# Kernel optimization log

Measured on AMD Instinct MI355X. Metric: run time of the kernel, lower is better.

The kernel has to match this reference:

```python
import jax, jax.numpy as jnp
import numpy as np

N = 60000      # total nodes
D = 300        # feature dim
R = 5          # num relations == num bases
E = 1_000_000  # edges
S = 25000      # last_idx_senses
G = 50000      # last_idx_globals
BATCH = 32


def setup_inputs() -> dict:
    key = jax.random.key(0)
    ks = jax.random.split(key, 12)
    x = jax.random.normal(ks[0], (N, D), dtype=jnp.float32)
    edge_index = jax.random.randint(ks[1], (2, E), 0, N, dtype=jnp.int32)
    edge_type = jax.random.randint(ks[2], (E,), 0, R, dtype=jnp.int32)
    current_node_index = jax.random.randint(ks[3], (BATCH,), 0, N, dtype=jnp.int32)
    scale = 1.0 / np.sqrt(D)
    # RGCNConv basis decomposition params (num_bases == num_relations)
    basis = jax.random.normal(ks[4], (R, D, D), dtype=jnp.float32) * scale
    comp = jax.random.normal(ks[5], (R, R), dtype=jnp.float32) * scale
    root = jax.random.normal(ks[6], (D, D), dtype=jnp.float32) * scale
    bias = jnp.zeros((D,), dtype=jnp.float32)
    # heads
    w_global = jax.random.normal(ks[7], (G - S, D), dtype=jnp.float32) * scale
    b_global = jnp.zeros((G - S,), dtype=jnp.float32)
    w_sense = jax.random.normal(ks[8], (S, D), dtype=jnp.float32) * scale
    b_sense = jnp.zeros((S,), dtype=jnp.float32)
    return {
        "x": x, "edge_index": edge_index, "edge_type": edge_type,
        "current_node_index": current_node_index,
        "basis": basis, "comp": comp, "root": root, "bias": bias,
        "w_global": w_global, "b_global": b_global,
        "w_sense": w_sense, "b_sense": b_sense,
    }


def reference(x, edge_index, edge_type, current_node_index,
              basis, comp, root, bias,
              w_global, b_global, w_sense, b_sense):
    src, dst = edge_index[0], edge_index[1]
    # Combined segment id over (dst node, relation): mean-aggregate source
    # features per (node, relation), then apply the per-relation transform
    # (mean(x_j) @ W_r == mean(x_j @ W_r); matches PyG RGCNConv aggr='mean').
    seg = dst * R + edge_type                      # [E]
    msg_sum = jax.ops.segment_sum(x[src], seg, num_segments=N * R)  # [N*R, D]
    cnt = jax.ops.segment_sum(jnp.ones((E,), jnp.float32), seg, num_segments=N * R)
    mean = msg_sum.reshape(N, R, D) / jnp.maximum(cnt.reshape(N, R, 1), 1.0)
    # basis decomposition: W_r = sum_b comp[r,b] * basis[b]
    W = jnp.einsum('rb,bij->rij', comp, basis)     # [R, D, D]
    agg = jnp.einsum('nrd,rde->ne', mean, W)       # [N, D]
    h = jax.nn.relu(agg + x @ root + bias)         # [N, D]
    hc = h[current_node_index]                     # [B, D]
    logits_global = hc @ w_global.T + b_global     # [B, G-S]
    logits_sense = hc @ w_sense.T + b_sense        # [B, S]
    return (jax.nn.log_softmax(logits_global, axis=-1),
            jax.nn.log_softmax(logits_sense, axis=-1))
```

## Files before the change

kernel.cpp:

```cpp
#include <hip/hip_runtime.h>
#include <hip/hip_bf16.h>
#include <math.h>

#define D 300
#define R 5
#define NE 1000000
#define B 32
#define NG 25000
#define NS 25000
#define NROWS 50000
#define NT16 3125
#define NBLK2 782
#define XQ 97
#define XR 6
#define HST 324

typedef __bf16 bf16x8 __attribute__((ext_vector_type(8)));
typedef float f32x4 __attribute__((ext_vector_type(4)));


__device__ __forceinline__ void online_upd(float& m, float& s, float v) {
    if (v > m) { s = s * __expf(m - v) + 1.0f; m = v; }
    else       { s += __expf(v - m); }
}
__device__ __forceinline__ void online_merge(float& m, float& s, float om, float os) {
    float M = fmaxf(m, om);
    s = s * __expf(m - M) + os * __expf(om - M);
    m = M;
}

__global__ void zero_ws(float4* __restrict__ p) {
    int i = blockIdx.x * 256 + threadIdx.x;
    if (i < 14440) p[i] = float4{0.f, 0.f, 0.f, 0.f};
}

__global__ __launch_bounds__(256) void scan_accum(
        const int* __restrict__ ei, const int* __restrict__ et,
        const int* __restrict__ cur, const float* __restrict__ x,
        float* __restrict__ wsum, float* __restrict__ wcnt) {
    __shared__ unsigned int tbl[32];
    __shared__ int curl[B];
    __shared__ int lcnt;
    __shared__ int2 loc[64];
    int tid = threadIdx.x;
    if (tid < 32) tbl[tid] = 0u;
    if (tid == 0) lcnt = 0;
    __syncthreads();
    if (tid < B) { int c = cur[tid]; curl[tid] = c; atomicOr(&tbl[(c >> 5) & 31], 1u << (c & 31)); }
    __syncthreads();
    long base = ((long)blockIdx.x * 256 + tid) * 4;
    if (base < NE) {
        int ds4[4];
        if (base + 4 <= NE) {
            int4 d4 = *(const int4*)(ei + NE + base);
            ds4[0] = d4.x; ds4[1] = d4.y; ds4[2] = d4.z; ds4[3] = d4.w;
        } else {
            for (int k = 0; k < 4; ++k) ds4[k] = (base + k < NE) ? ei[NE + base + k] : -1;
        }
        #pragma unroll
        for (int k = 0; k < 4; ++k) {
            int dst = ds4[k];
            if (dst < 0) continue;
            if (!(tbl[(dst >> 5) & 31] & (1u << (dst & 31)))) continue;
            int e = (int)base + k;
            int r = -1, src = 0;
            for (int b = 0; b < B; ++b) {
                if (dst == curl[b]) {
                    if (r < 0) { r = et[e]; src = ei[e]; }
                    atomicAdd(&wcnt[b * R + r], 1.0f);
                    int p = atomicAdd(&lcnt, 1);
                    if (p < 64) loc[p] = int2{src, b * R + r};
                }
            }
        }
    }
    __syncthreads();
    int n = lcnt; if (n > 64) n = 64;
    for (int m = 0; m < n; ++m) {
        int2 pr = loc[m];
        const float* xs = x + (long)pr.x * D;
        float* sm = wsum + (long)pr.y * D;
        for (int t = tid; t < D; t += 256) atomicAdd(&sm[t], xs[t]);
    }
}

__global__ __launch_bounds__(320) void rgcn_hc(
        const float* __restrict__ x, const int* __restrict__ cur,
        const float* __restrict__ comp, const float* __restrict__ root,
        const float* __restrict__ basis, const float* __restrict__ wsum,
        const float* __restrict__ wcnt, float* __restrict__ hcf) {
    int kc = blockIdx.x, t = threadIdx.x;
    __shared__ float uL[800];
    __shared__ float inv[B * R];
    __shared__ float cmp[R * R];
    if (t < B * R) inv[t] = 1.0f / fmaxf(wcnt[t], 1.0f);
    if (t >= 160 && t < 160 + R * R) cmp[t - 160] = comp[t - 160];
    __syncthreads();
    int d0 = kc * 25;
    if (d0 < 300) {
        for (int i = t; i < 800; i += 320) {
            int b = i / 25, dd = i - b * 25;
            uL[i] = x[(long)cur[b] * D + d0 + dd];
        }
    } else {
        int g0 = d0 - 300;
        int bb = g0 / 300, t0 = g0 - bb * 300;
        for (int i = t; i < 800; i += 320) {
            int b = i / 25, dd = i - b * 25;
            float a = 0.f;
            #pragma unroll
            for (int r = 0; r < R; ++r)
                a = fmaf(cmp[r * R + bb] * inv[b * R + r], wsum[(long)(b * R + r) * D + t0 + dd], a);
            uL[i] = a;
        }
    }
    __syncthreads();
    if (t < D) {
        const float* Mb = (d0 < 300) ? (root + (long)d0 * D) : (basis + (long)(d0 - 300) * D);
        float acc[B] = {};
        #pragma unroll 5
        for (int i = 0; i < 25; ++i) {
            float m = Mb[(long)i * D + t];
            #pragma unroll
            for (int b = 0; b < B; ++b) acc[b] = fmaf(uL[b * 25 + i], m, acc[b]);
        }
        for (int b = 0; b < B; ++b) atomicAdd(&hcf[b * D + t], acc[b]);
    }
}

__global__ __launch_bounds__(256) void head_gemm(
    const float* __restrict__ hcf, const float* __restrict__ bias,
    const float* __restrict__ wg, const float* __restrict__ bg,
    const float* __restrict__ wsn, const float* __restrict__ bsn,
    float* __restrict__ out, float2* __restrict__ pm2) {
    __shared__ __bf16 hcbL[32 * HST];
    __shared__ float2 sred[4][4][16];
    int tid = threadIdx.x;
    for (int i = tid; i < 32 * HST; i += 256) {
        int b = i / HST, kk = i - b * HST;
        float v = 0.f;
        if (kk < D) v = fmaxf(hcf[b * D + kk] + bias[kk], 0.f);
        hcbL[i] = (__bf16)v;
    }
    __syncthreads();

    int orig = blockIdx.x;
    int xcd = orig & 7, off = orig >> 3;
    int wgid = (xcd < XR ? xcd * (XQ + 1) : XR * (XQ + 1) + (xcd - XR) * XQ) + off;

    int wid = tid >> 6, l = tid & 63, ln = l & 15, og = l >> 4;
    int jt = wgid * 4 + wid;
    bool valid = jt < NT16;
    int jtc = valid ? jt : NT16 - 1;
    int jw = jtc * 16;
    int row = jw + ln;
    const float* wrow = ((row < NG) ? (wg + (long)row * D) : (wsn + (long)(row - NG) * D)) + og * 8;

    const __bf16* hrow0 = hcbL + ln * HST + og * 8;
    const __bf16* hrow1 = hcbL + (16 + ln) * HST + og * 8;
    f32x4 acc0 = {}, acc1 = {};
    #pragma unroll
    for (int s = 0; s < 9; ++s) {
        float4 w0 = *(const float4*)(wrow + 32 * s);
        float4 w1 = *(const float4*)(wrow + 32 * s + 4);
        bf16x8 a;
        a[0]=(__bf16)w0.x; a[1]=(__bf16)w0.y; a[2]=(__bf16)w0.z; a[3]=(__bf16)w0.w;
        a[4]=(__bf16)w1.x; a[5]=(__bf16)w1.y; a[6]=(__bf16)w1.z; a[7]=(__bf16)w1.w;
        acc0 = __builtin_amdgcn_mfma_f32_16x16x32_bf16(a, *(const bf16x8*)(hrow0 + 32 * s), acc0, 0, 0, 0);
        acc1 = __builtin_amdgcn_mfma_f32_16x16x32_bf16(a, *(const bf16x8*)(hrow1 + 32 * s), acc1, 0, 0, 0);
    }
    {
        float4 w0 = float4{0.f,0.f,0.f,0.f}, w1 = float4{0.f,0.f,0.f,0.f};
        if (og == 0) { w0 = *(const float4*)(wrow + 288); w1 = *(const float4*)(wrow + 292); }
        else if (og == 1) { w0 = *(const float4*)(wrow + 288); }
        bf16x8 a;
        a[0]=(__bf16)w0.x; a[1]=(__bf16)w0.y; a[2]=(__bf16)w0.z; a[3]=(__bf16)w0.w;
        a[4]=(__bf16)w1.x; a[5]=(__bf16)w1.y; a[6]=(__bf16)w1.z; a[7]=(__bf16)w1.w;
        acc0 = __builtin_amdgcn_mfma_f32_16x16x32_bf16(a, *(const bf16x8*)(hrow0 + 288), acc0, 0, 0, 0);
        acc1 = __builtin_amdgcn_mfma_f32_16x16x32_bf16(a, *(const bf16x8*)(hrow1 + 288), acc1, 0, 0, 0);
    }

    int b0 = ln, b1 = 16 + ln;
    float m0 = -3.0e38f, s0 = 0.f, m1 = -3.0e38f, s1 = 0.f;
    float m2 = -3.0e38f, s2 = 0.f, m3 = -3.0e38f, s3 = 0.f;
    if (valid) {
        #pragma unroll
        for (int r = 0; r < 4; ++r) {
            int j = jw + og * 4 + r;
            float bv = (j < NG) ? bg[j] : bsn[j - NG];
            float v0 = acc0[r] + bv;
            float v1 = acc1[r] + bv;
            float* op0 = (j < NG) ? (out + (long)b0 * NG + j)
                                  : (out + (long)B * NG + (long)b0 * NS + (j - NG));
            float* op1 = (j < NG) ? (out + (long)b1 * NG + j)
                                  : (out + (long)B * NG + (long)b1 * NS + (j - NG));
            *op0 = v0;
            *op1 = v1;
            if (j < NG) { online_upd(m0, s0, v0); online_upd(m2, s2, v1); }
            else        { online_upd(m1, s1, v0); online_upd(m3, s3, v1); }
        }
    }
    #pragma unroll
    for (int o = 16; o <= 32; o <<= 1) {
        float tm, ts;
        tm = __shfl_xor(m0, o); ts = __shfl_xor(s0, o); online_merge(m0, s0, tm, ts);
        tm = __shfl_xor(m1, o); ts = __shfl_xor(s1, o); online_merge(m1, s1, tm, ts);
        tm = __shfl_xor(m2, o); ts = __shfl_xor(s2, o); online_merge(m2, s2, tm, ts);
        tm = __shfl_xor(m3, o); ts = __shfl_xor(s3, o); online_merge(m3, s3, tm, ts);
    }
    if (l < 16) {
        sred[wid][0][ln] = float2{m0, s0};
        sred[wid][1][ln] = float2{m1, s1};
        sred[wid][2][ln] = float2{m2, s2};
        sred[wid][3][ln] = float2{m3, s3};
    }
    __syncthreads();
    if (tid < 64) {
        int k = tid >> 4, lnn = tid & 15;
        float m = -3.0e38f, s = 0.f;
        #pragma unroll
        for (int w = 0; w < 4; ++w) online_merge(m, s, sred[w][k][lnn].x, sred[w][k][lnn].y);
        int rw = (k & 1) * 32 + (k >> 1) * 16 + lnn;
        pm2[(long)rw * NBLK2 + wgid] = float2{m, s};
    }
}

__global__ __launch_bounds__(256) void lse_sub(float* __restrict__ out,
                                               const float2* __restrict__ pm2) {
    int rw = blockIdx.x / 25, c = blockIdx.x % 25;
    int tid = threadIdx.x;
    const float2* pr = pm2 + (long)rw * NBLK2;
    float m = -3.0e38f, s = 0.f;
    for (int i = tid; i < NBLK2; i += 256) { float2 e = pr[i]; online_merge(m, s, e.x, e.y); }
    #pragma unroll
    for (int o = 32; o; o >>= 1) {
        float om = __shfl_xor(m, o), os = __shfl_xor(s, o);
        online_merge(m, s, om, os);
    }
    __shared__ float sm[4], ss[4];
    __shared__ float lseS;
    if ((tid & 63) == 0) { sm[tid >> 6] = m; ss[tid >> 6] = s; }
    __syncthreads();
    if (tid == 0) {
        float M = sm[0], S = ss[0];
        for (int w = 1; w < 4; ++w) online_merge(M, S, sm[w], ss[w]);
        lseS = M + __logf(S);
    }
    __syncthreads();
    float l = lseS;
    float4* o4 = (float4*)out + (long)rw * 6250 + c * 250;
    if (tid < 250) { float4 v = o4[tid]; v.x -= l; v.y -= l; v.z -= l; v.w -= l; o4[tid] = v; }
}

extern "C" void kernel_launch(void* const* d_in, const int* in_sizes, int n_in,
                              void* d_out, int out_size, void* d_ws, size_t ws_size,
                              hipStream_t stream) {
    const float* x     = (const float*)d_in[0];
    const int*   ei    = (const int*)d_in[1];
    const int*   et    = (const int*)d_in[2];
    const int*   cur   = (const int*)d_in[3];
    const float* basis = (const float*)d_in[4];
    const float* comp  = (const float*)d_in[5];
    const float* root  = (const float*)d_in[6];
    const float* bias  = (const float*)d_in[7];
    const float* wg    = (const float*)d_in[8];
    const float* bgl   = (const float*)d_in[9];
    const float* wsn   = (const float*)d_in[10];
    const float* bsn   = (const float*)d_in[11];
    float* out  = (float*)d_out;
    float* wsf  = (float*)d_ws;
    float*  wsum = wsf;
    float*  wcnt = wsf + 48000;
    float*  hcf  = wsf + 48160;
    float2* pm2  = (float2*)(wsf + 57760);

    zero_ws<<<57, 256, 0, stream>>>((float4*)d_ws);
    scan_accum<<<977, 256, 0, stream>>>(ei, et, cur, x, wsum, wcnt);
    rgcn_hc<<<72, 320, 0, stream>>>(x, cur, comp, root, basis, wsum, wcnt, hcf);
    head_gemm<<<NBLK2, 256, 0, stream>>>(hcf, bias, wg, bgl, wsn, bsn, out, pm2);
    lse_sub<<<1600, 256, 0, stream>>>(out, pm2);
}
```

Before: 71.39 us.

## Stage head weights through LDS with coalesced loads and halve block size

The head GEMM now cooperatively loads each block's 32 weight rows into shared memory as bf16, using row-contiguous coalesced float4 loads. Previously each lane loaded its own strided fragment straight from global memory. Blocks shrink from four waves to two and the grid doubles, with the XCD remapping constants and the partial-LSE buffer stride updated to match. The aim is better global load efficiency and more blocks in flight. The cost is extra LDS traffic, a barrier before compute, and twice as many partial results for lse_sub to merge.

```diff
diff --git a/kernel.cpp b/kernel.cpp
--- a/kernel.cpp
+++ b/kernel.cpp
@@ -10,9 +10,9 @@
 #define NS 25000
 #define NROWS 50000
 #define NT16 3125
-#define NBLK2 782
-#define XQ 97
-#define XR 6
+#define NBLK2 1563
+#define XQ 195
+#define XR 3
 #define HST 324
 
 typedef __bf16 bf16x8 __attribute__((ext_vector_type(8)));
@@ -128,56 +128,55 @@
     }
 }
 
-__global__ __launch_bounds__(256) void head_gemm(
+__global__ __launch_bounds__(128) void head_gemm(
     const float* __restrict__ hcf, const float* __restrict__ bias,
     const float* __restrict__ wg, const float* __restrict__ bg,
     const float* __restrict__ wsn, const float* __restrict__ bsn,
     float* __restrict__ out, float2* __restrict__ pm2) {
     __shared__ __bf16 hcbL[32 * HST];
-    __shared__ float2 sred[4][4][16];
+    __shared__ __bf16 wtL[32 * HST];
+    __shared__ float2 sred[2][4][16];
     int tid = threadIdx.x;
-    for (int i = tid; i < 32 * HST; i += 256) {
-        int b = i / HST, kk = i - b * HST;
-        float v = 0.f;
-        if (kk < D) v = fmaxf(hcf[b * D + kk] + bias[kk], 0.f);
-        hcbL[i] = (__bf16)v;
-    }
-    __syncthreads();
 
     int orig = blockIdx.x;
     int xcd = orig & 7, off = orig >> 3;
     int wgid = (xcd < XR ? xcd * (XQ + 1) : XR * (XQ + 1) + (xcd - XR) * XQ) + off;
+    int r0 = wgid * 32;
+
+    for (int task = tid; task < 32 * 40; task += 128) {
+        int rr = task / 40, g = task - rr * 40;
+        int r = r0 + rr; if (r >= NROWS) r = NROWS - 1;
+        const float* wr = (r < NG) ? (wg + (long)r * D) : (wsn + (long)(r - NG) * D);
+        float4 w0 = float4{0.f,0.f,0.f,0.f}, w1 = float4{0.f,0.f,0.f,0.f};
+        if (g < 37)       { w0 = *(const float4*)(wr + g * 8); w1 = *(const float4*)(wr + g * 8 + 4); }
+        else if (g == 37) { w0 = *(const float4*)(wr + 296); }
+        bf16x8 a;
+        a[0]=(__bf16)w0.x; a[1]=(__bf16)w0.y; a[2]=(__bf16)w0.z; a[3]=(__bf16)w0.w;
+        a[4]=(__bf16)w1.x; a[5]=(__bf16)w1.y; a[6]=(__bf16)w1.z; a[7]=(__bf16)w1.w;
+        *(bf16x8*)(wtL + rr * HST + g * 8) = a;
+    }
+    for (int i = tid; i < 32 * 320; i += 128) {
+        int b = i >> 8; b = i / 320; int kk = i - b * 320;
+        float v = 0.f;
+        if (kk < D) v = fmaxf(hcf[b * D + kk] + bias[kk], 0.f);
+        hcbL[b * HST + kk] = (__bf16)v;
+    }
+    __syncthreads();
 
     int wid = tid >> 6, l = tid & 63, ln = l & 15, og = l >> 4;
-    int jt = wgid * 4 + wid;
+    int jt = wgid * 2 + wid;
     bool valid = jt < NT16;
-    int jtc = valid ? jt : NT16 - 1;
-    int jw = jtc * 16;
-    int row = jw + ln;
-    const float* wrow = ((row < NG) ? (wg + (long)row * D) : (wsn + (long)(row - NG) * D)) + og * 8;
-
+    int jw = (valid ? jt : NT16 - 1) * 16;
+
+    const __bf16* arow  = wtL + (wid * 16 + ln) * HST + og * 8;
     const __bf16* hrow0 = hcbL + ln * HST + og * 8;
     const __bf16* hrow1 = hcbL + (16 + ln) * HST + og * 8;
     f32x4 acc0 = {}, acc1 = {};
     #pragma unroll
-    for (int s = 0; s < 9; ++s) {
-        float4 w0 = *(const float4*)(wrow + 32 * s);
-        float4 w1 = *(const float4*)(wrow + 32 * s + 4);
-        bf16x8 a;
-        a[0]=(__bf16)w0.x; a[1]=(__bf16)w0.y; a[2]=(__bf16)w0.z; a[3]=(__bf16)w0.w;
-        a[4]=(__bf16)w1.x; a[5]=(__bf16)w1.y; a[6]=(__bf16)w1.z; a[7]=(__bf16)w1.w;
+    for (int s = 0; s < 10; ++s) {
+        bf16x8 a = *(const bf16x8*)(arow + 32 * s);
         acc0 = __builtin_amdgcn_mfma_f32_16x16x32_bf16(a, *(const bf16x8*)(hrow0 + 32 * s), acc0, 0, 0, 0);
         acc1 = __builtin_amdgcn_mfma_f32_16x16x32_bf16(a, *(const bf16x8*)(hrow1 + 32 * s), acc1, 0, 0, 0);
-    }
-    {
-        float4 w0 = float4{0.f,0.f,0.f,0.f}, w1 = float4{0.f,0.f,0.f,0.f};
-        if (og == 0) { w0 = *(const float4*)(wrow + 288); w1 = *(const float4*)(wrow + 292); }
-        else if (og == 1) { w0 = *(const float4*)(wrow + 288); }
-        bf16x8 a;
-        a[0]=(__bf16)w0.x; a[1]=(__bf16)w0.y; a[2]=(__bf16)w0.z; a[3]=(__bf16)w0.w;
-        a[4]=(__bf16)w1.x; a[5]=(__bf16)w1.y; a[6]=(__bf16)w1.z; a[7]=(__bf16)w1.w;
-        acc0 = __builtin_amdgcn_mfma_f32_16x16x32_bf16(a, *(const bf16x8*)(hrow0 + 288), acc0, 0, 0, 0);
-        acc1 = __builtin_amdgcn_mfma_f32_16x16x32_bf16(a, *(const bf16x8*)(hrow1 + 288), acc1, 0, 0, 0);
     }
 
     int b0 = ln, b1 = 16 + ln;
@@ -219,7 +218,7 @@
         int k = tid >> 4, lnn = tid & 15;
         float m = -3.0e38f, s = 0.f;
         #pragma unroll
-        for (int w = 0; w < 4; ++w) online_merge(m, s, sred[w][k][lnn].x, sred[w][k][lnn].y);
+        for (int w = 0; w < 2; ++w) online_merge(m, s, sred[w][k][lnn].x, sred[w][k][lnn].y);
         int rw = (k & 1) * 32 + (k >> 1) * 16 + lnn;
         pm2[(long)rw * NBLK2 + wgid] = float2{m, s};
     }
@@ -277,6 +276,6 @@
     zero_ws<<<57, 256, 0, stream>>>((float4*)d_ws);
     scan_accum<<<977, 256, 0, stream>>>(ei, et, cur, x, wsum, wcnt);
     rgcn_hc<<<72, 320, 0, stream>>>(x, cur, comp, root, basis, wsum, wcnt, hcf);
-    head_gemm<<<NBLK2, 256, 0, stream>>>(hcf, bias, wg, bgl, wsn, bsn, out, pm2);
+    head_gemm<<<NBLK2, 128, 0, stream>>>(hcf, bias, wg, bgl, wsn, bsn, out, pm2);
     lse_sub<<<1600, 256, 0, stream>>>(out, pm2);
 }
```

Measured after the change: 140.8 us. +97.2%, slower.
